# Optimization experiments

Hardware: AMD Instinct MI355X
Metric: run time of the kernel (lower is better)

## Reference

```python
import jax, jax.numpy as jnp
import numpy as np

SOS, EOS = 0, 1
MAXLEN = 128
EPS = 1e-5


def setup_inputs() -> dict:
    key = jax.random.key(0)
    ks = jax.random.split(key, 10)
    B, T, Hc, Hs, V, Hm = 64, 1024, 512, 512, 64, 128
    h = jax.random.normal(ks[0], (B, T, Hc), dtype=jnp.float32)
    x_seq_lens = jax.random.randint(ks[1], (B,), 1, T + 1).astype(jnp.int32)
    s = 0.05
    return {
        "h": h,
        "W_ih": jax.random.normal(ks[2], (4 * Hs, V + Hc), dtype=jnp.float32) * s,
        "W_hh": jax.random.normal(ks[3], (4 * Hs, Hs), dtype=jnp.float32) * s,
        "b_ih": jax.random.normal(ks[4], (4 * Hs,), dtype=jnp.float32) * s,
        "b_hh": jax.random.normal(ks[5], (4 * Hs,), dtype=jnp.float32) * s,
        "fc1_w": jax.random.normal(ks[6], (Hm, Hs + Hc), dtype=jnp.float32) * s,
        "fc1_b": jax.random.normal(ks[7], (Hm,), dtype=jnp.float32) * s,
        "fc2_w": jax.random.normal(ks[8], (V, Hm), dtype=jnp.float32) * s,
        "x_seq_lens": x_seq_lens,
    }


def reference(h, W_ih, W_hh, b_ih, b_hh, fc1_w, fc1_b, fc2_w, x_seq_lens):
    B, T, Hc = h.shape
    Hs = W_hh.shape[1]
    V = fc2_w.shape[0]
    # attention length mask [B, T]
    mask = (jnp.arange(T)[None, :] < x_seq_lens[:, None]).astype(h.dtype)
    sos = jax.nn.one_hot(jnp.full((B,), SOS), V, dtype=h.dtype)
    x0 = jnp.concatenate([sos, h[:, 0, :]], axis=-1)  # [B, V+Hc]
    carry0 = (x0, jnp.zeros((B, Hs), h.dtype), jnp.zeros((B, Hs), h.dtype),
              jnp.full((B,), MAXLEN, jnp.int32))

    def step(carry, t):
        x, hs, cs, lens = carry
        # single-layer LSTM cell, torch gate order i,f,g,o
        gates = x @ W_ih.T + hs @ W_hh.T + b_ih + b_hh
        i, f, g, o = jnp.split(gates, 4, axis=-1)
        cs = jax.nn.sigmoid(f) * cs + jax.nn.sigmoid(i) * jnp.tanh(g)
        hs = jax.nn.sigmoid(o) * jnp.tanh(cs)
        # dot-product attention (apply_proj=False, num_heads=1)
        e = jnp.einsum('bd,btd->bt', hs, h)
        exps = jnp.exp(e - jnp.max(e)) * mask  # MaskedSoftmax: global-max shift
        a = exps / (exps.sum(-1, keepdims=True) + EPS)
        ctx = jnp.einsum('bt,btd->bd', a, h)
        # chardist: two stacked linears (no nonlinearity), then softmax
        feat = jnp.concatenate([hs, ctx], axis=-1)
        logits = (feat @ fc1_w.T + fc1_b) @ fc2_w.T
        y_hat = jax.nn.softmax(logits, axis=-1)
        hit = (jnp.argmax(y_hat, axis=-1) == EOS) & (lens > t)
        lens = jnp.where(hit, t + 1, lens)
        x = jnp.concatenate([y_hat, ctx], axis=-1)  # decode mode (y=None)
        return (x, hs, cs, lens), (y_hat, a)

    (_, _, _, lens), (y_hats, atts) = jax.lax.scan(step, carry0, jnp.arange(MAXLEN))
    y_hats = jnp.transpose(y_hats, (1, 0, 2))              # [B, L, V]
    attentions = jnp.transpose(atts, (1, 0, 2))[:, None]   # [B, 1, L, T]
    return y_hats, lens, attentions
```

## Files before the change

### kernel.cpp

```cpp
#include <hip/hip_runtime.h>
#include <math.h>

typedef unsigned short ushort_t;
typedef unsigned int uint_t;

#define OFF_XT    0
#define OFF_CS    102400
#define OFF_E     135168
#define OFF_MD    200704
#define OFF_LENS  204800
#define OFF_W2    204864
#define OFF_B2    270400
#define OFF_CP    270464
#define OFF_HB16F 1319040
#define WS_NEED   ((size_t)(1319040 + 16777216) * 4)

#define OUT_YH   0
#define OUT_LENS 524288
#define OUT_ATT  524352

__device__ __forceinline__ float sigf(float x) { return 1.0f / (1.0f + __expf(-x)); }
__device__ __forceinline__ float dot4(float4 a, float4 b) {
    return a.x * b.x + a.y * b.y + a.z * b.z + a.w * b.w;
}
__device__ __forceinline__ uint_t bf16rne(float x) {
    uint_t u = __float_as_uint(x);
    return (u + 0x7FFFu + ((u >> 16) & 1u)) >> 16;
}
#define BLO(u) __uint_as_float((u) << 16)
#define BHI(u) __uint_as_float((u) & 0xFFFF0000u)

__global__ void k_init(const float* __restrict__ h, float* __restrict__ ws) {
    int blk = blockIdx.x, tid = threadIdx.x;
    int idx = blk * 256 + tid;
    if (idx < 102400) {
        int k = idx >> 6, b = idx & 63;
        float v = 0.0f;
        if (k == 0) v = 1.0f;
        else if (k >= 64 && k < 576) v = h[(size_t)b * 524288 + (k - 64)];
        ws[OFF_XT + idx] = v;
    }
    if (blk >= 400 && blk < 528)
        ws[OFF_CS + (blk - 400) * 256 + tid] = 0.0f;
    if (blk == 527 && tid < 64) ((int*)ws)[OFF_LENS + tid] = 128;
}

__global__ void k_hconv(const float* __restrict__ h, float* __restrict__ ws) {
    size_t i = ((size_t)blockIdx.x * 256 + threadIdx.x) * 8;
    float4 a = *(const float4*)(h + i);
    float4 b = *(const float4*)(h + i + 4);
    uint4 o;
    o.x = bf16rne(a.x) | (bf16rne(a.y) << 16);
    o.y = bf16rne(a.z) | (bf16rne(a.w) << 16);
    o.z = bf16rne(b.x) | (bf16rne(b.y) << 16);
    o.w = bf16rne(b.z) | (bf16rne(b.w) << 16);
    *(uint4*)((ushort_t*)(ws + OFF_HB16F) + i) = o;
}

__global__ void k_fuse(const float* __restrict__ fc1w, const float* __restrict__ fc1b,
                       const float* __restrict__ fc2w, float* __restrict__ ws) {
    int blk = blockIdx.x;
    int v = blk >> 2, kc = blk & 3;
    int k = kc * 256 + threadIdx.x;
    float acc = 0.0f;
#pragma unroll 8
    for (int m = 0; m < 128; m++) acc += fc2w[v * 128 + m] * fc1w[(size_t)m * 1024 + k];
    ws[OFF_W2 + (size_t)v * 1024 + k] = acc;
    if (kc == 0 && threadIdx.x == 0) {
        float bb = 0.0f;
        for (int m = 0; m < 128; m++) bb += fc2w[v * 128 + m] * fc1b[m];
        ws[OFF_B2 + v] = bb;
    }
}

__global__ void k_gates(const float* __restrict__ Wih, const float* __restrict__ Whh,
                        const float* __restrict__ bih, const float* __restrict__ bhh,
                        float* __restrict__ ws, int p) {
    const int tid = threadIdx.x;
    const int lane = tid & 63;
    const int w = tid >> 6;
    const int hs_in  = 576 + (p ? 512 : 0);
    const int hs_out = 576 + (p ? 0 : 512);
    __shared__ float gpart[4096];
    const int u0 = blockIdx.x * 2;
    const int wq = __builtin_amdgcn_readfirstlane(w);
    float acc[2][4] = {{0, 0, 0, 0}, {0, 0, 0, 0}};
    int k0 = wq * 136, k1 = k0 + 136;
    int kx1 = k1 < 576 ? k1 : 576;
#pragma unroll 2
    for (int k = k0; k < kx1; k += 4) {
        float4 xv;
        xv.x = ws[OFF_XT + (k + 0) * 64 + lane];
        xv.y = ws[OFF_XT + (k + 1) * 64 + lane];
        xv.z = ws[OFF_XT + (k + 2) * 64 + lane];
        xv.w = ws[OFF_XT + (k + 3) * 64 + lane];
#pragma unroll
        for (int uu = 0; uu < 2; ++uu)
#pragma unroll
            for (int g = 0; g < 4; ++g)
                acc[uu][g] += dot4(*(const float4*)&Wih[(size_t)(g * 512 + u0 + uu) * 576 + k], xv);
    }
    int kh0 = k0 > 576 ? k0 : 576;
#pragma unroll 2
    for (int k = kh0; k < k1; k += 4) {
        float4 xv;
        xv.x = ws[OFF_XT + (hs_in + (k - 576) + 0) * 64 + lane];
        xv.y = ws[OFF_XT + (hs_in + (k - 576) + 1) * 64 + lane];
        xv.z = ws[OFF_XT + (hs_in + (k - 576) + 2) * 64 + lane];
        xv.w = ws[OFF_XT + (hs_in + (k - 576) + 3) * 64 + lane];
#pragma unroll
        for (int uu = 0; uu < 2; ++uu)
#pragma unroll
            for (int g = 0; g < 4; ++g)
                acc[uu][g] += dot4(*(const float4*)&Whh[(size_t)(g * 512 + u0 + uu) * 512 + (k - 576)], xv);
    }
#pragma unroll
    for (int uu = 0; uu < 2; ++uu)
#pragma unroll
        for (int g = 0; g < 4; ++g)
            gpart[((w * 2 + uu) * 4 + g) * 64 + lane] = acc[uu][g];
    __syncthreads();
    if (tid < 128) {
        int uu = tid >> 6, b = tid & 63;
        int u = u0 + uu;
        float g4[4];
#pragma unroll
        for (int g = 0; g < 4; ++g) {
            float s = 0.0f;
#pragma unroll
            for (int ww = 0; ww < 8; ++ww) s += gpart[((ww * 2 + uu) * 4 + g) * 64 + b];
            g4[g] = s + bih[g * 512 + u] + bhh[g * 512 + u];
        }
        int idx = u * 64 + b;
        float co = ws[OFF_CS + idx];
        float I = sigf(g4[0]), F = sigf(g4[1]), G = tanhf(g4[2]), O = sigf(g4[3]);
        float cn = F * co + I * G;
        ws[OFF_CS + idx] = cn;
        ws[OFF_XT + (size_t)(hs_out + u) * 64 + b] = O * tanhf(cn);
    }
}

__global__ void k_attn16(const int* __restrict__ slen, float* __restrict__ ws, int p) {
    const int blk = blockIdx.x;
    const int tid = threadIdx.x;
    const int lane = tid & 63;
    const int w = tid >> 6;
    const int hs_out = 576 + (p ? 0 : 512);
    const int b = blk >> 5, sb = blk & 31;
    const int L = slen[b];
    const int t0 = sb * 32;
    __shared__ ushort_t stage[16384];
    __shared__ float hs_sh[512];
    __shared__ float e_sh[32];
    __shared__ float wt_sh[32];
    const ushort_t* hb = (const ushort_t*)(ws + OFF_HB16F) + ((size_t)b * 1024 + t0) * 512;
    uint4 r0 = *(const uint4*)(hb + 0 * 2048 + tid * 8);
    uint4 r1 = *(const uint4*)(hb + 1 * 2048 + tid * 8);
    uint4 r2 = *(const uint4*)(hb + 2 * 2048 + tid * 8);
    uint4 r3 = *(const uint4*)(hb + 3 * 2048 + tid * 8);
    uint4 r4 = *(const uint4*)(hb + 4 * 2048 + tid * 8);
    uint4 r5 = *(const uint4*)(hb + 5 * 2048 + tid * 8);
    uint4 r6 = *(const uint4*)(hb + 6 * 2048 + tid * 8);
    uint4 r7 = *(const uint4*)(hb + 7 * 2048 + tid * 8);
    hs_sh[tid]       = ws[OFF_XT + (size_t)(hs_out + tid) * 64 + b];
    hs_sh[256 + tid] = ws[OFF_XT + (size_t)(hs_out + 256 + tid) * 64 + b];
    __syncthreads();
    float hsv[8];
#pragma unroll
    for (int j = 0; j < 8; ++j) hsv[j] = hs_sh[lane * 8 + j];
#define EROW(J, R)                                                                  \
    {                                                                               \
        float part = BLO(R.x) * hsv[0] + BHI(R.x) * hsv[1]                          \
                   + BLO(R.y) * hsv[2] + BHI(R.y) * hsv[3]                          \
                   + BLO(R.z) * hsv[4] + BHI(R.z) * hsv[5]                          \
                   + BLO(R.w) * hsv[6] + BHI(R.w) * hsv[7];                         \
        _Pragma("unroll")                                                           \
        for (int mm = 1; mm < 64; mm <<= 1) part += __shfl_xor(part, mm);           \
        if (lane == 0) e_sh[4 * (J) + w] = part;                                    \
        *(uint4*)&stage[(J) * 2048 + tid * 8] = R;                                  \
    }
    EROW(0, r0) EROW(1, r1) EROW(2, r2) EROW(3, r3)
    EROW(4, r4) EROW(5, r5) EROW(6, r6) EROW(7, r7)
#undef EROW
    __syncthreads();
    float m_reg = 0.0f;
    if (tid < 32) {
        float m = e_sh[0];
#pragma unroll
        for (int j = 1; j < 32; ++j) m = fmaxf(m, e_sh[j]);
        m_reg = m;
        int tg = t0 + tid;
        wt_sh[tid] = (tg < L) ? __expf(e_sh[tid] - m) : 0.0f;
        ws[OFF_E + (size_t)b * 1024 + t0 + tid] = e_sh[tid];
    }
    __syncthreads();
    int nr = L - t0;
    nr = nr < 0 ? 0 : (nr > 32 ? 32 : nr);
    float accx = 0.0f, accy = 0.0f;
    const uint_t* st32 = (const uint_t*)stage;
    for (int tl = 0; tl < nr; ++tl) {
        float wt = wt_sh[tl];
        uint_t v = st32[tl * 256 + tid];
        accx += wt * BLO(v);
        accy += wt * BHI(v);
    }
    float2 o2; o2.x = accx; o2.y = accy;
    *(float2*)&ws[OFF_CP + (size_t)(b * 32 + sb) * 512 + tid * 2] = o2;
    if (tid == 0) {
        float D = 0.0f;
#pragma unroll
        for (int tl = 0; tl < 32; ++tl) D += wt_sh[tl];
        ws[OFF_MD + (b * 32 + sb) * 2]     = m_reg;
        ws[OFF_MD + (b * 32 + sb) * 2 + 1] = D;
    }
}

__global__ void k_attn(const float* __restrict__ h, const int* __restrict__ slen,
                       float* __restrict__ ws, int p) {
    const int blk = blockIdx.x;
    const int tid = threadIdx.x;
    const int lane = tid & 63;
    const int w = tid >> 6;
    const int hs_out = 576 + (p ? 0 : 512);
    const int b = blk >> 4, sb = blk & 15;
    const int L = slen[b];
    const int t0 = sb * 64;
    __shared__ float stage[4096];
    __shared__ float hs_sh[512];
    __shared__ float e_sh[8];
    const float* hb = h + ((size_t)b * 1024 + t0) * 512;
    hs_sh[tid]       = ws[OFF_XT + (size_t)(hs_out + tid) * 64 + b];
    hs_sh[256 + tid] = ws[OFF_XT + (size_t)(hs_out + 256 + tid) * 64 + b];
    __syncthreads();
    float hsv[8];
#pragma unroll
    for (int j = 0; j < 8; ++j) hsv[j] = hs_sh[lane * 8 + j];
    float m_run = -INFINITY, D = 0.0f, accx = 0.0f, accy = 0.0f;
    for (int c = 0; c < 8; ++c) {
        const float* gsrc = hb + (size_t)c * 4096 + tid * 4;
        float4 tv0 = *(const float4*)(gsrc);
        float4 tv1 = *(const float4*)(gsrc + 1024);
        float4 tv2 = *(const float4*)(gsrc + 2048);
        float4 tv3 = *(const float4*)(gsrc + 3072);
        __syncthreads();
        *(float4*)&stage[tid * 4]        = tv0;
        *(float4*)&stage[1024 + tid * 4] = tv1;
        *(float4*)&stage[2048 + tid * 4] = tv2;
        *(float4*)&stage[3072 + tid * 4] = tv3;
        __syncthreads();
#pragma unroll
        for (int rr = 0; rr < 2; ++rr) {
            int tl = w * 2 + rr;
            const float4* rp = (const float4*)&stage[tl * 512 + lane * 8];
            float4 pp = rp[0], qq = rp[1];
            float part = pp.x * hsv[0] + pp.y * hsv[1] + pp.z * hsv[2] + pp.w * hsv[3]
                       + qq.x * hsv[4] + qq.y * hsv[5] + qq.z * hsv[6] + qq.w * hsv[7];
#pragma unroll
            for (int mm = 1; mm < 64; mm <<= 1) part += __shfl_xor(part, mm);
            if (lane == 0) {
                e_sh[tl] = part;
                ws[OFF_E + (size_t)b * 1024 + t0 + c * 8 + tl] = part;
            }
        }
        __syncthreads();
        float cm = e_sh[0];
#pragma unroll
        for (int j = 1; j < 8; ++j) cm = fmaxf(cm, e_sh[j]);
        float m_new = fmaxf(m_run, cm);
        float sc = __expf(m_run - m_new);
        accx *= sc; accy *= sc; D *= sc;
        m_run = m_new;
#pragma unroll
        for (int tl = 0; tl < 8; ++tl) {
            int tg = t0 + c * 8 + tl;
            float wt = (tg < L) ? __expf(e_sh[tl] - m_run) : 0.0f;
            D += wt;
            float2 hv = *(const float2*)&stage[tl * 512 + tid * 2];
            accx += wt * hv.x;
            accy += wt * hv.y;
        }
    }
    float2 o2; o2.x = accx; o2.y = accy;
    *(float2*)&ws[OFF_CP + (size_t)(b * 16 + sb) * 512 + tid * 2] = o2;
    if (tid == 0) {
        ws[OFF_MD + (b * 16 + sb) * 2]     = m_run;
        ws[OFF_MD + (b * 16 + sb) * 2 + 1] = D;
    }
}

__global__ void k_comb(const int* __restrict__ slen, float* __restrict__ ws,
                       float* __restrict__ out, int p, int ts, int ns) {
    const int b = blockIdx.x, tid = threadIdx.x;
    const int hs_out = 576 + (p ? 0 : 512);
    __shared__ float red[256];
    __shared__ float feat[1024];
    __shared__ float sc_sh[32];
    __shared__ float lg_s[64];
    const int nent = 64 * ns;
    float mx = -INFINITY;
    for (int i = tid; i < nent; i += 256) mx = fmaxf(mx, ws[OFF_MD + i * 2]);
    red[tid] = mx;
    __syncthreads();
    for (int s = 128; s > 0; s >>= 1) {
        if (tid < s) red[tid] = fmaxf(red[tid], red[tid + s]);
        __syncthreads();
    }
    float m_g = red[0];
    __syncthreads();
    if (tid < ns) {
        float mi = ws[OFF_MD + (b * ns + tid) * 2];
        float Di = ws[OFF_MD + (b * ns + tid) * 2 + 1];
        float s = __expf(mi - m_g);
        sc_sh[tid] = s;
        red[tid] = s * Di;
    }
    __syncthreads();
    float dn = 0.0f;
    for (int j = 0; j < ns; ++j) dn += red[j];
    float inv = 1.0f / (dn + 1e-5f);
    float cx = 0.0f, cy = 0.0f;
    for (int i = 0; i < ns; ++i) {
        float s = sc_sh[i];
        float2 v = *(const float2*)&ws[OFF_CP + (size_t)(b * ns + i) * 512 + tid * 2];
        cx += s * v.x;
        cy += s * v.y;
    }
    cx *= inv; cy *= inv;
    feat[512 + tid * 2] = cx;
    feat[512 + tid * 2 + 1] = cy;
    ws[OFF_XT + (size_t)(64 + tid * 2) * 64 + b] = cx;
    ws[OFF_XT + (size_t)(64 + tid * 2 + 1) * 64 + b] = cy;
    feat[tid * 2]     = ws[OFF_XT + (size_t)(hs_out + tid * 2) * 64 + b];
    feat[tid * 2 + 1] = ws[OFF_XT + (size_t)(hs_out + tid * 2 + 1) * 64 + b];
    int L = slen[b];
#pragma unroll
    for (int q = 0; q < 4; ++q) {
        int t = tid + 256 * q;
        float e = ws[OFF_E + (size_t)b * 1024 + t];
        float a = (t < L) ? __expf(e - m_g) * inv : 0.0f;
        out[OUT_ATT + (size_t)b * 131072 + (size_t)ts * 1024 + t] = a;
    }
    __syncthreads();
    int v = tid >> 2, qq = tid & 3;
    const float4* w4 = (const float4*)(ws + OFF_W2 + (size_t)v * 1024 + qq * 256);
    const float4* f4 = (const float4*)feat + qq * 64;
    float acc = 0.0f;
#pragma unroll 8
    for (int k = 0; k < 64; ++k) acc += dot4(w4[k], f4[k]);
    acc += __shfl_xor(acc, 1);
    acc += __shfl_xor(acc, 2);
    if (qq == 0) lg_s[v] = acc;
    __syncthreads();
    if (tid < 64) {
        float lg = lg_s[tid] + ws[OFF_B2 + tid];
        float mxv = lg;
#pragma unroll
        for (int mm = 1; mm < 64; mm <<= 1) mxv = fmaxf(mxv, __shfl_xor(mxv, mm));
        float ev = __expf(lg - mxv);
        float s = ev;
#pragma unroll
        for (int mm = 1; mm < 64; mm <<= 1) s += __shfl_xor(s, mm);
        float y = ev / s;
        out[OUT_YH + (size_t)b * 8192 + ts * 64 + tid] = y;
        ws[OFF_XT + (size_t)tid * 64 + b] = y;
        float av = lg;
        int ai = tid;
#pragma unroll
        for (int mm = 1; mm < 64; mm <<= 1) {
            float ov = __shfl_xor(av, mm);
            int oi = __shfl_xor(ai, mm);
            if (ov > av || (ov == av && oi < ai)) { av = ov; ai = oi; }
        }
        if (tid == 0) {
            int* lens = (int*)ws + OFF_LENS;
            if (ai == 1 && lens[b] > ts) lens[b] = ts + 1;
            if (ts == 127) out[OUT_LENS + b] = (float)lens[b];
        }
    }
}

extern "C" void kernel_launch(void* const* d_in, const int* in_sizes, int n_in,
                              void* d_out, int out_size, void* d_ws, size_t ws_size,
                              hipStream_t stream) {
    (void)in_sizes; (void)n_in; (void)out_size;
    const float* h    = (const float*)d_in[0];
    const float* Wih  = (const float*)d_in[1];
    const float* Whh  = (const float*)d_in[2];
    const float* bih  = (const float*)d_in[3];
    const float* bhh  = (const float*)d_in[4];
    const float* fc1w = (const float*)d_in[5];
    const float* fc1b = (const float*)d_in[6];
    const float* fc2w = (const float*)d_in[7];
    const int*   slen = (const int*)d_in[8];
    float* ws  = (float*)d_ws;
    float* out = (float*)d_out;
    const bool use16 = (ws_size >= WS_NEED);
    const int ns = use16 ? 32 : 16;

    k_init<<<528, 256, 0, stream>>>(h, ws);
    k_fuse<<<256, 256, 0, stream>>>(fc1w, fc1b, fc2w, ws);
    if (use16) k_hconv<<<16384, 256, 0, stream>>>(h, ws);
    for (int t = 0; t < 128; t++) {
        int p = t & 1;
        k_gates<<<256, 512, 0, stream>>>(Wih, Whh, bih, bhh, ws, p);
        if (use16) k_attn16<<<2048, 256, 0, stream>>>(slen, ws, p);
        else       k_attn<<<1024, 256, 0, stream>>>(h, slen, ws, p);
        k_comb<<<64, 256, 0, stream>>>(slen, ws, out, p, t, ns);
    }
}
```

Measured before the change: 6.536 ms.

## Fuse attention combine into attention kernel via last-block atomic counter

Merges the per-step combine kernel into the bf16 attention kernel. Every block bumps a per-timestep atomic counter, and the blocks with the last sub-block index spin until all 2048 blocks have arrived, then do the global max, context reduction, logits, softmax and lens update. The block index mapping is changed so those final blocks are scheduled last. This removes one kernel launch per step, but adds a spin-wait that depends on all blocks being resident or already finished, which risks deadlock or stalls.

```diff
diff --git a/kernel.cpp b/kernel.cpp
--- a/kernel.cpp
+++ b/kernel.cpp
@@ -9,11 +9,12 @@
 #define OFF_E     135168
 #define OFF_MD    200704
 #define OFF_LENS  204800
-#define OFF_W2    204864
-#define OFF_B2    270400
-#define OFF_CP    270464
-#define OFF_HB16F 1319040
-#define WS_NEED   ((size_t)(1319040 + 16777216) * 4)
+#define OFF_CTR   204864
+#define OFF_W2    204992
+#define OFF_B2    270528
+#define OFF_CP    270592
+#define OFF_HB16F 1319168
+#define WS_NEED   ((size_t)(1319168 + 16777216) * 4)
 
 #define OUT_YH   0
 #define OUT_LENS 524288
@@ -42,7 +43,10 @@
     }
     if (blk >= 400 && blk < 528)
         ws[OFF_CS + (blk - 400) * 256 + tid] = 0.0f;
-    if (blk == 527 && tid < 64) ((int*)ws)[OFF_LENS + tid] = 128;
+    if (blk == 527) {
+        if (tid < 64) ((int*)ws)[OFF_LENS + tid] = 128;
+        if (tid >= 64 && tid < 192) ((int*)ws)[OFF_CTR + tid - 64] = 0;
+    }
 }
 
 __global__ void k_hconv(const float* __restrict__ h, float* __restrict__ ws) {
@@ -140,19 +144,21 @@
     }
 }
 
-__global__ void k_attn16(const int* __restrict__ slen, float* __restrict__ ws, int p) {
+__global__ void k_attn_comb(const int* __restrict__ slen, float* __restrict__ ws,
+                            float* __restrict__ out, int p, int ts) {
     const int blk = blockIdx.x;
     const int tid = threadIdx.x;
     const int lane = tid & 63;
     const int w = tid >> 6;
     const int hs_out = 576 + (p ? 0 : 512);
-    const int b = blk >> 5, sb = blk & 31;
+    const int sb = blk >> 6, b = blk & 63;
     const int L = slen[b];
     const int t0 = sb * 32;
-    __shared__ ushort_t stage[16384];
+    __shared__ uint4 stage4[2048];
     __shared__ float hs_sh[512];
     __shared__ float e_sh[32];
     __shared__ float wt_sh[32];
+    ushort_t* stage = (ushort_t*)stage4;
     const ushort_t* hb = (const ushort_t*)(ws + OFF_HB16F) + ((size_t)b * 1024 + t0) * 512;
     uint4 r0 = *(const uint4*)(hb + 0 * 2048 + tid * 8);
     uint4 r1 = *(const uint4*)(hb + 1 * 2048 + tid * 8);
@@ -212,6 +218,103 @@
         for (int tl = 0; tl < 32; ++tl) D += wt_sh[tl];
         ws[OFF_MD + (b * 32 + sb) * 2]     = m_reg;
         ws[OFF_MD + (b * 32 + sb) * 2 + 1] = D;
+    }
+    __syncthreads();
+    int* ctr = (int*)ws + OFF_CTR + ts;
+    if (tid == 0)
+        __hip_atomic_fetch_add(ctr, 1, __ATOMIC_RELEASE, __HIP_MEMORY_SCOPE_AGENT);
+    if (sb != 31) return;
+
+    if (tid == 0) {
+        while (__hip_atomic_load(ctr, __ATOMIC_ACQUIRE, __HIP_MEMORY_SCOPE_AGENT) < 2048)
+            __builtin_amdgcn_s_sleep(8);
+    }
+    __syncthreads();
+    float* red   = (float*)stage4;
+    float* feat  = (float*)stage4 + 256;
+    float* sc_sh = (float*)stage4 + 1280;
+    float* lg_s  = (float*)stage4 + 1312;
+    float mx = -INFINITY;
+#pragma unroll
+    for (int i = 0; i < 8; ++i) mx = fmaxf(mx, ws[OFF_MD + (tid + 256 * i) * 2]);
+    red[tid] = mx;
+    __syncthreads();
+    for (int s = 128; s > 0; s >>= 1) {
+        if (tid < s) red[tid] = fmaxf(red[tid], red[tid + s]);
+        __syncthreads();
+    }
+    float m_g = red[0];
+    __syncthreads();
+    if (tid < 32) {
+        float mi = ws[OFF_MD + (b * 32 + tid) * 2];
+        float Di = ws[OFF_MD + (b * 32 + tid) * 2 + 1];
+        float s = __expf(mi - m_g);
+        sc_sh[tid] = s;
+        red[tid] = s * Di;
+    }
+    __syncthreads();
+    float dn = 0.0f;
+#pragma unroll
+    for (int j = 0; j < 32; ++j) dn += red[j];
+    float inv = 1.0f / (dn + 1e-5f);
+    float cx = 0.0f, cy = 0.0f;
+#pragma unroll 4
+    for (int i = 0; i < 32; ++i) {
+        float s = sc_sh[i];
+        float2 v = *(const float2*)&ws[OFF_CP + (size_t)(b * 32 + i) * 512 + tid * 2];
+        cx += s * v.x;
+        cy += s * v.y;
+    }
+    cx *= inv; cy *= inv;
+    feat[512 + tid * 2] = cx;
+    feat[512 + tid * 2 + 1] = cy;
+    ws[OFF_XT + (size_t)(64 + tid * 2) * 64 + b] = cx;
+    ws[OFF_XT + (size_t)(64 + tid * 2 + 1) * 64 + b] = cy;
+    feat[tid * 2]     = ws[OFF_XT + (size_t)(hs_out + tid * 2) * 64 + b];
+    feat[tid * 2 + 1] = ws[OFF_XT + (size_t)(hs_out + tid * 2 + 1) * 64 + b];
+#pragma unroll
+    for (int q = 0; q < 4; ++q) {
+        int t = tid + 256 * q;
+        float e = ws[OFF_E + (size_t)b * 1024 + t];
+        float a = (t < L) ? __expf(e - m_g) * inv : 0.0f;
+        out[OUT_ATT + (size_t)b * 131072 + (size_t)ts * 1024 + t] = a;
+    }
+    __syncthreads();
+    int v = tid >> 2, qq = tid & 3;
+    const float4* w4 = (const float4*)(ws + OFF_W2 + (size_t)v * 1024 + qq * 256);
+    const float4* f4 = (const float4*)feat + qq * 64;
+    float acc = 0.0f;
+#pragma unroll 8
+    for (int k = 0; k < 64; ++k) acc += dot4(w4[k], f4[k]);
+    acc += __shfl_xor(acc, 1);
+    acc += __shfl_xor(acc, 2);
+    if (qq == 0) lg_s[v] = acc;
+    __syncthreads();
+    if (tid < 64) {
+        float lg = lg_s[tid] + ws[OFF_B2 + tid];
+        float mxv = lg;
+#pragma unroll
+        for (int mm = 1; mm < 64; mm <<= 1) mxv = fmaxf(mxv, __shfl_xor(mxv, mm));
+        float ev = __expf(lg - mxv);
+        float s = ev;
+#pragma unroll
+        for (int mm = 1; mm < 64; mm <<= 1) s += __shfl_xor(s, mm);
+        float y = ev / s;
+        out[OUT_YH + (size_t)b * 8192 + ts * 64 + tid] = y;
+        ws[OFF_XT + (size_t)tid * 64 + b] = y;
+        float av = lg;
+        int ai = tid;
+#pragma unroll
+        for (int mm = 1; mm < 64; mm <<= 1) {
+            float ov = __shfl_xor(av, mm);
+            int oi = __shfl_xor(ai, mm);
+            if (ov > av || (ov == av && oi < ai)) { av = ov; ai = oi; }
+        }
+        if (tid == 0) {
+            int* lens = (int*)ws + OFF_LENS;
+            if (ai == 1 && lens[b] > ts) lens[b] = ts + 1;
+            if (ts == 127) out[OUT_LENS + b] = (float)lens[b];
+        }
     }
 }
 
@@ -395,7 +498,6 @@
     float* ws  = (float*)d_ws;
     float* out = (float*)d_out;
     const bool use16 = (ws_size >= WS_NEED);
-    const int ns = use16 ? 32 : 16;
 
     k_init<<<528, 256, 0, stream>>>(h, ws);
     k_fuse<<<256, 256, 0, stream>>>(fc1w, fc1b, fc2w, ws);
@@ -403,8 +505,11 @@
     for (int t = 0; t < 128; t++) {
         int p = t & 1;
         k_gates<<<256, 512, 0, stream>>>(Wih, Whh, bih, bhh, ws, p);
-        if (use16) k_attn16<<<2048, 256, 0, stream>>>(slen, ws, p);
-        else       k_attn<<<1024, 256, 0, stream>>>(h, slen, ws, p);
-        k_comb<<<64, 256, 0, stream>>>(slen, ws, out, p, t, ns);
-    }
-}
+        if (use16) {
+            k_attn_comb<<<2048, 256, 0, stream>>>(slen, ws, out, p, t);
+        } else {
+            k_attn<<<1024, 256, 0, stream>>>(h, slen, ws, p);
+            k_comb<<<64, 256, 0, stream>>>(slen, ws, out, p, t, 16);
+        }
+    }
+}
```

New measurement: 13.90 ms. +112.7%, slower.

## Keep attention rows in registers and widen gate K-split to 16 waves

Applied to the files above, without the earlier changes.

The attention kernel now keeps each thread's bf16 h slice in registers and reuses it for the weighted context sum. Each 16-lane group reduces a column slice, so the LDS staging buffer and the serial per-row loop are gone. Partial scores are combined across waves through a small shared array. The gates kernel doubles its block size to 1024 threads, halving each wave's K range and enlarging the shared partial buffer. This trades more reduction work and shuffles for less LDS traffic and more parallelism.

```diff
diff --git a/kernel.cpp b/kernel.cpp
--- a/kernel.cpp
+++ b/kernel.cpp
@@ -73,19 +73,20 @@
     }
 }
 
-__global__ void k_gates(const float* __restrict__ Wih, const float* __restrict__ Whh,
-                        const float* __restrict__ bih, const float* __restrict__ bhh,
-                        float* __restrict__ ws, int p) {
+__global__ __launch_bounds__(1024) void k_gates(
+        const float* __restrict__ Wih, const float* __restrict__ Whh,
+        const float* __restrict__ bih, const float* __restrict__ bhh,
+        float* __restrict__ ws, int p) {
     const int tid = threadIdx.x;
     const int lane = tid & 63;
     const int w = tid >> 6;
     const int hs_in  = 576 + (p ? 512 : 0);
     const int hs_out = 576 + (p ? 0 : 512);
-    __shared__ float gpart[4096];
+    __shared__ float gpart[8192];
     const int u0 = blockIdx.x * 2;
     const int wq = __builtin_amdgcn_readfirstlane(w);
     float acc[2][4] = {{0, 0, 0, 0}, {0, 0, 0, 0}};
-    int k0 = wq * 136, k1 = k0 + 136;
+    int k0 = wq * 68, k1 = k0 + 68;
     int kx1 = k1 < 576 ? k1 : 576;
 #pragma unroll 2
     for (int k = k0; k < kx1; k += 4) {
@@ -128,7 +129,7 @@
         for (int g = 0; g < 4; ++g) {
             float s = 0.0f;
 #pragma unroll
-            for (int ww = 0; ww < 8; ++ww) s += gpart[((ww * 2 + uu) * 4 + g) * 64 + b];
+            for (int ww = 0; ww < 16; ++ww) s += gpart[((ww * 2 + uu) * 4 + g) * 64 + b];
             g4[g] = s + bih[g * 512 + u] + bhh[g * 512 + u];
         }
         int idx = u * 64 + b;
@@ -140,77 +141,96 @@
     }
 }
 
-__global__ void k_attn16(const int* __restrict__ slen, float* __restrict__ ws, int p) {
+__global__ __launch_bounds__(256) void k_attn16(const int* __restrict__ slen,
+                                                float* __restrict__ ws, int p) {
     const int blk = blockIdx.x;
     const int tid = threadIdx.x;
     const int lane = tid & 63;
-    const int w = tid >> 6;
+    const int w = __builtin_amdgcn_readfirstlane(tid >> 6);
+    const int rg = lane >> 4, cl = lane & 15;
     const int hs_out = 576 + (p ? 0 : 512);
     const int b = blk >> 5, sb = blk & 31;
     const int L = slen[b];
     const int t0 = sb * 32;
-    __shared__ ushort_t stage[16384];
     __shared__ float hs_sh[512];
+    __shared__ float e_part[128];
     __shared__ float e_sh[32];
     __shared__ float wt_sh[32];
-    const ushort_t* hb = (const ushort_t*)(ws + OFF_HB16F) + ((size_t)b * 1024 + t0) * 512;
-    uint4 r0 = *(const uint4*)(hb + 0 * 2048 + tid * 8);
-    uint4 r1 = *(const uint4*)(hb + 1 * 2048 + tid * 8);
-    uint4 r2 = *(const uint4*)(hb + 2 * 2048 + tid * 8);
-    uint4 r3 = *(const uint4*)(hb + 3 * 2048 + tid * 8);
-    uint4 r4 = *(const uint4*)(hb + 4 * 2048 + tid * 8);
-    uint4 r5 = *(const uint4*)(hb + 5 * 2048 + tid * 8);
-    uint4 r6 = *(const uint4*)(hb + 6 * 2048 + tid * 8);
-    uint4 r7 = *(const uint4*)(hb + 7 * 2048 + tid * 8);
+    const ushort_t* hb = (const ushort_t*)(ws + OFF_HB16F)
+                       + ((size_t)b * 1024 + t0) * 512 + w * 128 + cl * 8;
+    uint4 r0 = *(const uint4*)(hb + (size_t)(rg * 8 + 0) * 512);
+    uint4 r1 = *(const uint4*)(hb + (size_t)(rg * 8 + 1) * 512);
+    uint4 r2 = *(const uint4*)(hb + (size_t)(rg * 8 + 2) * 512);
+    uint4 r3 = *(const uint4*)(hb + (size_t)(rg * 8 + 3) * 512);
+    uint4 r4 = *(const uint4*)(hb + (size_t)(rg * 8 + 4) * 512);
+    uint4 r5 = *(const uint4*)(hb + (size_t)(rg * 8 + 5) * 512);
+    uint4 r6 = *(const uint4*)(hb + (size_t)(rg * 8 + 6) * 512);
+    uint4 r7 = *(const uint4*)(hb + (size_t)(rg * 8 + 7) * 512);
     hs_sh[tid]       = ws[OFF_XT + (size_t)(hs_out + tid) * 64 + b];
     hs_sh[256 + tid] = ws[OFF_XT + (size_t)(hs_out + 256 + tid) * 64 + b];
     __syncthreads();
     float hsv[8];
 #pragma unroll
-    for (int j = 0; j < 8; ++j) hsv[j] = hs_sh[lane * 8 + j];
+    for (int j = 0; j < 8; ++j) hsv[j] = hs_sh[w * 128 + cl * 8 + j];
 #define EROW(J, R)                                                                  \
     {                                                                               \
         float part = BLO(R.x) * hsv[0] + BHI(R.x) * hsv[1]                          \
                    + BLO(R.y) * hsv[2] + BHI(R.y) * hsv[3]                          \
                    + BLO(R.z) * hsv[4] + BHI(R.z) * hsv[5]                          \
                    + BLO(R.w) * hsv[6] + BHI(R.w) * hsv[7];                         \
-        _Pragma("unroll")                                                           \
-        for (int mm = 1; mm < 64; mm <<= 1) part += __shfl_xor(part, mm);           \
-        if (lane == 0) e_sh[4 * (J) + w] = part;                                    \
-        *(uint4*)&stage[(J) * 2048 + tid * 8] = R;                                  \
+        part += __shfl_xor(part, 1);                                                \
+        part += __shfl_xor(part, 2);                                                \
+        part += __shfl_xor(part, 4);                                                \
+        part += __shfl_xor(part, 8);                                                \
+        if (cl == 0) e_part[w * 32 + rg * 8 + (J)] = part;                          \
     }
     EROW(0, r0) EROW(1, r1) EROW(2, r2) EROW(3, r3)
     EROW(4, r4) EROW(5, r5) EROW(6, r6) EROW(7, r7)
 #undef EROW
     __syncthreads();
-    float m_reg = 0.0f;
+    if (tid < 32) {
+        float e = e_part[tid] + e_part[32 + tid] + e_part[64 + tid] + e_part[96 + tid];
+        e_sh[tid] = e;
+        ws[OFF_E + (size_t)b * 1024 + t0 + tid] = e;
+    }
+    __syncthreads();
     if (tid < 32) {
         float m = e_sh[0];
 #pragma unroll
         for (int j = 1; j < 32; ++j) m = fmaxf(m, e_sh[j]);
-        m_reg = m;
         int tg = t0 + tid;
         wt_sh[tid] = (tg < L) ? __expf(e_sh[tid] - m) : 0.0f;
-        ws[OFF_E + (size_t)b * 1024 + t0 + tid] = e_sh[tid];
-    }
-    __syncthreads();
-    int nr = L - t0;
-    nr = nr < 0 ? 0 : (nr > 32 ? 32 : nr);
-    float accx = 0.0f, accy = 0.0f;
-    const uint_t* st32 = (const uint_t*)stage;
-    for (int tl = 0; tl < nr; ++tl) {
-        float wt = wt_sh[tl];
-        uint_t v = st32[tl * 256 + tid];
-        accx += wt * BLO(v);
-        accy += wt * BHI(v);
-    }
-    float2 o2; o2.x = accx; o2.y = accy;
-    *(float2*)&ws[OFF_CP + (size_t)(b * 32 + sb) * 512 + tid * 2] = o2;
+        if (tid == 0) ws[OFF_MD + (b * 32 + sb) * 2] = m;
+    }
+    __syncthreads();
+    float acc[8] = {0, 0, 0, 0, 0, 0, 0, 0};
+#define PVROW(J, R)                                                                 \
+    {                                                                               \
+        float wt = wt_sh[rg * 8 + (J)];                                             \
+        acc[0] += wt * BLO(R.x); acc[1] += wt * BHI(R.x);                           \
+        acc[2] += wt * BLO(R.y); acc[3] += wt * BHI(R.y);                           \
+        acc[4] += wt * BLO(R.z); acc[5] += wt * BHI(R.z);                           \
+        acc[6] += wt * BLO(R.w); acc[7] += wt * BHI(R.w);                           \
+    }
+    PVROW(0, r0) PVROW(1, r1) PVROW(2, r2) PVROW(3, r3)
+    PVROW(4, r4) PVROW(5, r5) PVROW(6, r6) PVROW(7, r7)
+#undef PVROW
+#pragma unroll
+    for (int k = 0; k < 8; ++k) {
+        acc[k] += __shfl_xor(acc[k], 16);
+        acc[k] += __shfl_xor(acc[k], 32);
+    }
+    if (rg == 0) {
+        float4 o0; o0.x = acc[0]; o0.y = acc[1]; o0.z = acc[2]; o0.w = acc[3];
+        float4 o1; o1.x = acc[4]; o1.y = acc[5]; o1.z = acc[6]; o1.w = acc[7];
+        float* cp = ws + OFF_CP + (size_t)(b * 32 + sb) * 512 + w * 128 + cl * 8;
+        *(float4*)cp = o0;
+        *(float4*)(cp + 4) = o1;
+    }
     if (tid == 0) {
         float D = 0.0f;
 #pragma unroll
         for (int tl = 0; tl < 32; ++tl) D += wt_sh[tl];
-        ws[OFF_MD + (b * 32 + sb) * 2]     = m_reg;
         ws[OFF_MD + (b * 32 + sb) * 2 + 1] = D;
     }
 }
@@ -395,16 +415,19 @@
     float* ws  = (float*)d_ws;
     float* out = (float*)d_out;
     const bool use16 = (ws_size >= WS_NEED);
-    const int ns = use16 ? 32 : 16;
 
     k_init<<<528, 256, 0, stream>>>(h, ws);
     k_fuse<<<256, 256, 0, stream>>>(fc1w, fc1b, fc2w, ws);
     if (use16) k_hconv<<<16384, 256, 0, stream>>>(h, ws);
     for (int t = 0; t < 128; t++) {
         int p = t & 1;
-        k_gates<<<256, 512, 0, stream>>>(Wih, Whh, bih, bhh, ws, p);
-        if (use16) k_attn16<<<2048, 256, 0, stream>>>(slen, ws, p);
-        else       k_attn<<<1024, 256, 0, stream>>>(h, slen, ws, p);
-        k_comb<<<64, 256, 0, stream>>>(slen, ws, out, p, t, ns);
-    }
-}
+        k_gates<<<256, 1024, 0, stream>>>(Wih, Whh, bih, bhh, ws, p);
+        if (use16) {
+            k_attn16<<<2048, 256, 0, stream>>>(slen, ws, p);
+            k_comb<<<64, 256, 0, stream>>>(slen, ws, out, p, t, 32);
+        } else {
+            k_attn<<<1024, 256, 0, stream>>>(h, slen, ws, p);
+            k_comb<<<64, 256, 0, stream>>>(slen, ws, out, p, t, 16);
+        }
+    }
+}
```

Result: faster. 6.112 ms (-6.5%).
